# Optimization experiments

Hardware: AMD Instinct MI355X
Metric: run time of the kernel (lower is better)

The kernel has to match this reference:

```python
import jax, jax.numpy as jnp
import numpy as np

V = 32000; D = 1024; L = 2; H = 16; KVH = 4; HD = D // H; E = 8; FF = 2048; K = 2
B = 2; S = 1024; WINDOW = 4096; THETA = 10000.0; EPS = 1e-6


def setup_inputs() -> dict:
    key = jax.random.key(0)
    ks = jax.random.split(key, 12)
    std = 0.02
    return {
        'tokens': jax.random.randint(ks[0], (B, S), 0, V),
        'tok_emb': jax.random.normal(ks[1], (V, D), jnp.float32),  # nn.Embedding default N(0,1)
        'norm1_w': jnp.ones((L, D), jnp.float32),
        'norm2_w': jnp.ones((L, D), jnp.float32),
        'wq': jax.random.normal(ks[2], (L, D, D), jnp.float32) * std,
        'wk': jax.random.normal(ks[3], (L, KVH * HD, D), jnp.float32) * std,
        'wv': jax.random.normal(ks[4], (L, KVH * HD, D), jnp.float32) * std,
        'wo': jax.random.normal(ks[5], (L, D, D), jnp.float32) * std,
        'router_w': jax.random.normal(ks[6], (L, E, D), jnp.float32) * (std / np.sqrt(D)),
        'w1': jax.random.normal(ks[7], (L, E, FF, D), jnp.float32) * std,
        'w2': jax.random.normal(ks[8], (L, E, FF, D), jnp.float32) * std,
        'w3': jax.random.normal(ks[9], (L, E, D, FF), jnp.float32) * std,
        'normf_w': jnp.ones((D,), jnp.float32),
        'head_w': jax.random.normal(ks[10], (V, D), jnp.float32) * std,
    }


def rmsnorm(x, w):
    # F.normalize(x, dim=-1, eps) * w * sqrt(d)
    n = jnp.linalg.norm(x, axis=-1, keepdims=True)
    return x / jnp.maximum(n, EPS) * w * np.float32(np.sqrt(x.shape[-1]))


def rope(x, cos, sin):
    # x: (b, s, h, hd); pairs are interleaved (even, odd) per view_as_complex
    x2 = x.reshape(x.shape[:-1] + (-1, 2))
    x0, x1 = x2[..., 0], x2[..., 1]
    o0 = x0 * cos - x1 * sin
    o1 = x0 * sin + x1 * cos
    return jnp.stack([o0, o1], axis=-1).reshape(x.shape)


def attention(x, wq, wk, wv, wo, cos, sin):
    b, s, _ = x.shape
    q = (x @ wq.T).reshape(b, s, H, HD)
    k = (x @ wk.T).reshape(b, s, KVH, HD)
    v = (x @ wv.T).reshape(b, s, KVH, HD)
    q = rope(q, cos, sin)
    k = rope(k, cos, sin)
    g = H // KVH
    k = jnp.repeat(k, g, axis=2)
    v = jnp.repeat(v, g, axis=2)
    scores = jnp.einsum('bqhd,bkhd->bhqk', q, k) / np.float32(np.sqrt(HD))
    i = jnp.arange(s)[:, None]; j = jnp.arange(s)[None, :]
    allow = (j <= i) & (i - j < WINDOW)  # causal + sliding window
    scores = jnp.where(allow, scores, -jnp.inf)
    attn = jax.nn.softmax(scores, axis=-1)
    out = jnp.einsum('bhqk,bkhd->bqhd', attn, v).reshape(b, s, D)
    return out @ wo.T


def moe(x, router_w, w1, w2, w3):
    b, s, d = x.shape
    logits = jnp.einsum('bsd,ed->bse', x, router_w)
    probs = jax.nn.softmax(logits, axis=-1)
    _, idx = jax.lax.top_k(probs, K)                      # (b, s, K)
    mask = jax.nn.one_hot(idx, E, dtype=x.dtype).sum(-2)  # (b, s, E) binary
    xt = x.reshape(-1, d)           # (T, d)
    mt = mask.reshape(-1, E)        # (T, E)
    # Dense masked dispatch: every expert computed on all tokens, combine masks to zero
    u = jnp.einsum('td,efd->etf', xt, w1)
    g = jax.nn.silu(u) * jnp.einsum('td,efd->etf', xt, w2)
    y = jnp.einsum('etf,edf->etd', g, w3)
    out = jnp.einsum('etd,te->td', y, mt).reshape(b, s, d)  # unweighted combine (per source)
    # aux losses
    z_loss = jnp.mean(jax.scipy.special.logsumexp(logits, axis=-1)) ** 2
    load = probs.sum(axis=0)  # (s, E), matching probs.sum(dim=0) in source
    load_loss = (jnp.std(load, ddof=1) / jnp.mean(load)) ** 2
    aux = 0.001 * z_loss + 0.001 * load_loss
    return out, aux


def _rope_tables(dtype):
    freqs = 1.0 / (THETA ** (np.arange(0, HD, 2, dtype=np.float32) / HD))
    ang = np.arange(S, dtype=np.float32)[:, None] * freqs[None, :]
    cos = jnp.asarray(np.cos(ang), dtype)[None, :, None, :]
    sin = jnp.asarray(np.sin(ang), dtype)[None, :, None, :]
    return cos, sin


def reference(tokens, tok_emb, norm1_w, norm2_w, wq, wk, wv, wo, router_w, w1, w2, w3, normf_w, head_w):
    x = tok_emb[tokens]  # (B, S, D)
    cos, sin = _rope_tables(x.dtype)
    attn_scale = np.float32(1.0 / np.sqrt(2.0 * L))
    aux_total = jnp.zeros((), x.dtype)
    for l in range(L):
        x = x + attn_scale * attention(rmsnorm(x, norm1_w[l]), wq[l], wk[l], wv[l], wo[l], cos, sin)
        mo, aux = moe(rmsnorm(x, norm2_w[l]), router_w[l], w1[l], w2[l], w3[l])
        x = x + mo
        aux_total = aux_total + aux
    logits = rmsnorm(x, normf_w) @ head_w.T
    return logits, aux_total
```

## Files before the change

### kernel.cpp

```cpp
#include <hip/hip_runtime.h>
#include <math.h>

#define DEV __device__ __forceinline__

using v8s = __attribute__((ext_vector_type(8))) short;
using v4f = __attribute__((ext_vector_type(4))) float;

DEV short f2bf(float f) {
    unsigned u = __float_as_uint(f);
    unsigned r = (u + 0x7fffu + ((u >> 16) & 1u)) >> 16;
    return (short)(unsigned short)r;
}
DEV float bf2f(short s) {
    return __uint_as_float(((unsigned)(unsigned short)s) << 16);
}

DEV void gload16(const short* g, short* l) {
    __builtin_amdgcn_global_load_lds((const __attribute__((address_space(1))) void*)g,
                                     (__attribute__((address_space(3))) void*)l,
                                     16, 0, 0);
}

DEV void raw_barrier() { asm volatile("s_barrier" ::: "memory"); }

// ... 43 lines not shown
                                                     (unsigned short)l6, (unsigned short)l7);
        }
    }
}

struct GemmP {
    const short* Ah; const short* Al;
    const short* Bh; const short* Bl;
    float* C; short* Ch; short* Cl;
    const int* cnt; const int* ppd; const int* lrow;
    long aPanelsZ;
    long strideAz;
    long strideBz, strideCz;
    int M, N, K, lda, ldc;
    float alpha;
    int outMode;
    int gqaB;
    int grouped;
    int causalSkip;
    int causalK;
    int ntiles, S, G;
};

template<bool SPLIT, bool AREG>
__global__ __launch_bounds__(256) void gemm_bt(GemmP p) {
    const int lid = blockIdx.x;
    const int xcd = lid & 7, sI = lid >> 3;
    const int gi = xcd + 8 * (sI / p.S);
    if (gi >= p.G) return;
    const int mt = sI % p.S;
    const int nt = gi % p.ntiles;
    const int z  = gi / p.ntiles;
    if (p.causalSkip && nt > mt) return;

    const int tid = threadIdx.x;

    int Mz = p.grouped ? p.cnt[z] : p.M;
    if (mt * 128 >= Mz) return;

    long bOff;
    if (p.gqaB) { int b = z >> 4, h = z & 15; bOff = (long)(b * 4 + (h >> 2)) * p.strideBz; }
    else bOff = (long)z * p.strideBz;

    extern __shared__ char smem[];
    short* s0 = (short*)smem;
    const int BUF = SPLIT ? 16384 : 8192;

    const int lane = tid & 63, w = tid >> 6;
    const int lr = lane & 15, lg = lane >> 4;
    const int wr = w >> 1, wc = w & 1;

    v4f acc[4][4];
#pragma unroll
    for (int i = 0; i < 4; ++i)
#pragma unroll
        for (int j = 0; j < 4; ++j) { acc[i][j][0] = 0.f; acc[i][j][1] = 0.f; acc[i][j][2] = 0.f; acc[i][j][3] = 0.f; }

    const short* bks  = p.Bh + bOff + (long)nt * 128 * p.K + (long)w * 1024 + lane * 8;
    const short* bksL = SPLIT ? p.Bl + bOff + (long)nt * 128 * p.K + (long)w * 1024 + lane * 8 : nullptr;

    const short *aks = nullptr, *aksL = nullptr;
    const short *aH = nullptr, *aL = nullptr;
    short *sA0 = nullptr, *sA1 = nullptr, *sA0l = nullptr, *sA1l = nullptr;
    if constexpr (AREG) {
        const int r = tid & 127;
        const int kgA = tid >> 7;
        int am = mt * 128 + r; if (am >= Mz) am = Mz - 1;
        long arowoff = (long)z * p.strideAz + (long)am * p.lda;
        aH = p.Ah + arowoff + kgA * 16;
        aL = SPLIT ? p.Al + arowoff + kgA * 16 : nullptr;
        sA0 = s0 + (kgA * 256 + r) * 8; sA1 = sA0 + 1024;
        sA0l = s0 + 8192 + (kgA * 256 + r) * 8; sA1l = sA0l + 1024;
    } else {
        long aPanel = (p.grouped ? (long)(p.ppd[z] >> 7) : (long)z * p.aPanelsZ) + mt;
        aks  = p.Ah + aPanel * 128L * p.K + (long)w * 1024 + lane * 8;
        aksL = SPLIT ? p.Al + aPanel * 128L * p.K + (long)w * 1024 + lane * 8 : nullptr;
    }

    const int kEnd = p.causalK ? min(p.K, (mt + 1) * 128) : p.K;

    if constexpr (!AREG) {
        const int nIter = kEnd >> 5;
        const int wb = w * 1024;
        {
            const long kb = 0;
            short* base = s0;
            gload16(aks + kb,       base + wb);
            gload16(aks + kb + 512, base + wb + 512);
            gload16(bks + kb,       base + 4096 + wb);
            gload16(bks + kb + 512, base + 4096 + wb + 512);
            if (SPLIT) {
                gload16(aksL + kb,       base + 8192 + wb);
                gload16(aksL + kb + 512, base + 8192 + wb + 512);
                gload16(bksL + kb,       base + 12288 + wb);
                gload16(bksL + kb + 512, base + 12288 + wb + 512);
            }
        }
        for (int i = 0; i < nIter; ++i) {
            const int cur = i & 1;
            if (i + 1 < nIter) {
                raw_barrier();
                const long kb = (long)(i + 1) * 4096;
                short* base = s0 + (cur ^ 1) * BUF;
                gload16(aks + kb,       base + wb);
                gload16(aks + kb + 512, base + wb + 512);
                gload16(bks + kb,       base + 4096 + wb);
                gload16(bks + kb + 512, base + 4096 + wb + 512);
                if (SPLIT) {
                    gload16(aksL + kb,       base + 8192 + wb);
                    gload16(aksL + kb + 512, base + 8192 + wb + 512);
                    gload16(bksL + kb,       base + 12288 + wb);
                    gload16(bksL + kb + 512, base + 12288 + wb + 512);
                }
                if constexpr (SPLIT) asm volatile("s_waitcnt vmcnt(8)" ::: "memory");
                else                 asm volatile("s_waitcnt vmcnt(4)" ::: "memory");
            } else {
                asm volatile("s_waitcnt vmcnt(0)" ::: "memory");
            }
            raw_barrier();
            const short* base = s0 + cur * BUF;
            const int abase = lg * 1024 + (wr * 64 + lr) * 8;
            const int bbase = 4096 + lg * 1024 + (wc * 64 + lr) * 8;
            v8s ah[4], bh[4];
#pragma unroll
            for (int q = 0; q < 4; ++q) {
                ah[q] = *(const v8s*)(base + abase + q * 128);
                bh[q] = *(const v8s*)(base + bbase + q * 128);
            }
            if constexpr (SPLIT) {
                v8s al[4], bl[4];
#pragma unroll
                for (int q = 0; q < 4; ++q) {
                    al[q] = *(const v8s*)(base + 8192 + abase + q * 128);
                    bl[q] = *(const v8s*)(base + 8192 + bbase + q * 128);
                }
#pragma unroll
                for (int mi = 0; mi < 4; ++mi)
#pragma unroll
                    for (int nj = 0; nj < 4; ++nj) {
                        acc[mi][nj] = __builtin_amdgcn_mfma_f32_16x16x32_bf16(ah[mi], bh[nj], acc[mi][nj], 0, 0, 0);
                        acc[mi][nj] = __builtin_amdgcn_mfma_f32_16x16x32_bf16(al[mi], bh[nj], acc[mi][nj], 0, 0, 0);
                        acc[mi][nj] = __builtin_amdgcn_mfma_f32_16x16x32_bf16(ah[mi], bl[nj], acc[mi][nj], 0, 0, 0);
                    }
            } else {
#pragma unroll
                for (int mi = 0; mi < 4; ++mi)
#pragma unroll
                    for (int nj = 0; nj < 4; ++nj)
                        acc[mi][nj] = __builtin_amdgcn_mfma_f32_16x16x32_bf16(ah[mi], bh[nj], acc[mi][nj], 0, 0, 0);
            }
        }
    } else {
        short* Ahs = s0;
        short* Bhs = s0 + 4096;
        short* Als = s0 + 8192;
        short* Bls = s0 + 12288;
        const int wb = w * 1024;
        for (int k0 = 0; k0 < kEnd; k0 += 32) {
            const long kb = (long)k0 * 128;
            uint4 a0 = *(const uint4*)(aH + k0);
            uint4 a1 = *(const uint4*)(aH + k0 + 8);
            uint4 a0l, a1l;
            if (SPLIT) { a0l = *(const uint4*)(aL + k0); a1l = *(const uint4*)(aL + k0 + 8); }
            __syncthreads();
            gload16(bks + kb,       Bhs + wb);
            gload16(bks + kb + 512, Bhs + wb + 512);
            if (SPLIT) {
                gload16(bksL + kb,       Bls + wb);
                gload16(bksL + kb + 512, Bls + wb + 512);
            }
            *(uint4*)sA0 = a0; *(uint4*)sA1 = a1;
            if (SPLIT) { *(uint4*)sA0l = a0l; *(uint4*)sA1l = a1l; }
            __syncthreads();
            const int abase = lg * 1024 + (wr * 64 + lr) * 8;
            const int bbase = lg * 1024 + (wc * 64 + lr) * 8;
            v8s ah[4], bh[4];
#pragma unroll
            for (int q = 0; q < 4; ++q) {
                ah[q] = *(const v8s*)(Ahs + abase + q * 128);
                bh[q] = *(const v8s*)(Bhs + bbase + q * 128);
            }
            if constexpr (SPLIT) {
                v8s al[4], bl[4];
#pragma unroll
                for (int q = 0; q < 4; ++q) {
                    al[q] = *(const v8s*)(Als + abase + q * 128);
                    bl[q] = *(const v8s*)(Bls + bbase + q * 128);
                }
#pragma unroll
                for (int mi = 0; mi < 4; ++mi)
#pragma unroll
                    for (int nj = 0; nj < 4; ++nj) {
                        acc[mi][nj] = __builtin_amdgcn_mfma_f32_16x16x32_bf16(ah[mi], bh[nj], acc[mi][nj], 0, 0, 0);
                        acc[mi][nj] = __builtin_amdgcn_mfma_f32_16x16x32_bf16(al[mi], bh[nj], acc[mi][nj], 0, 0, 0);
                        acc[mi][nj] = __builtin_amdgcn_mfma_f32_16x16x32_bf16(ah[mi], bl[nj], acc[mi][nj], 0, 0, 0);
                    }
            } else {
#pragma unroll
                for (int mi = 0; mi < 4; ++mi)
#pragma unroll
                    for (int nj = 0; nj < 4; ++nj)
                        acc[mi][nj] = __builtin_amdgcn_mfma_f32_16x16x32_bf16(ah[mi], bh[nj], acc[mi][nj], 0, 0, 0);
            }
        }
    }

#pragma unroll
    for (int mi = 0; mi < 4; ++mi) {
        const int mrow = mt * 128 + wr * 64 + mi * 16 + lg * 4;
#pragma unroll
        for (int nj = 0; nj < 4; ++nj) {
            const int ncol = nt * 128 + wc * 64 + nj * 16 + lr;
            if (ncol < p.N) {
#pragma unroll
                for (int rr = 0; rr < 4; ++rr) {
                    const int m = mrow + rr;
                    if (m < Mz) {
                        float v = acc[mi][nj][rr] * p.alpha;
                        if (p.outMode == 3) {
                            int b = z >> 4, h = z & 15;
                            int grow = b * 1024 + m, col = h * 64 + ncol;
                            long dst = ((long)(grow >> 7)) * 131072 + ((long)(col >> 5) << 12)
                                     + ((long)((col >> 3) & 3) << 10) + ((long)(grow & 127) << 3) + (col & 7);
                            short hi = f2bf(v);
                            p.Ch[dst] = hi;
                            p.Cl[dst] = f2bf(v - bf2f(hi));
                        } else {
                            long crow;
                            if (p.grouped == 1)      crow = p.ppd[z] + m;
                            else if (p.grouped == 2) crow = p.lrow[z * 2048 + m];
                            else                     crow = m;
                            long co = (long)z * p.strideCz + crow * (long)p.ldc + ncol;
                            if (p.outMode == 0) p.C[co] = v;
                            else                p.C[co] += v;
                        }
                    }
                }
            }
        }
    }
}

__global__ __launch_bounds__(256) void embed_kernel(const int* toks, const float* emb, float* X) {
    const int t = blockIdx.x;
    const int tok = toks[t];
    const float4* s = (const float4*)(emb + (size_t)tok * 1024);
    float4* d = (float4*)(X + (size_t)t * 1024);
    d[threadIdx.x] = s[threadIdx.x];
}

__global__ __launch_bounds__(256) void rmsnorm_split(const float* X, const float* w, short* oh, short* ol) {
    __shared__ float red[4];
    const long t = blockIdx.x;
    const float* r = X + t * 1024;
    float ss = 0.f;
    for (int j = threadIdx.x; j < 1024; j += 256) { float f = r[j]; ss += f * f; }
    ss = block_sum256(ss, red);
    const float sc = 32.f / fmaxf(sqrtf(ss), 1e-6f);
    if (threadIdx.x < 128) {
// ... 45 lines not shown
    short h0 = f2bf(o0); KH[off] = h0; KL[off] = f2bf(o0 - bf2f(h0));
    short h1 = f2bf(o1); KH[off + 1] = h1; KL[off + 1] = f2bf(o1 - bf2f(h1));
}

__global__ __launch_bounds__(256) void transpose_v_kernel(const float* QKV, short* VH, short* VL) {
    const int idx = blockIdx.x * 256 + threadIdx.x;
    const int d = idx & 63, kv = (idx >> 6) & 3, s = (idx >> 8) & 1023, b = idx >> 18;
    const float f = QKV[((size_t)(b * 1024 + s)) * 1536 + 1280 + kv * 64 + d];
    const int z = b * 4 + kv;
    const long off = (long)z * 131072 + ((long)(s >> 5) << 12) + ((long)((s >> 3) & 3) << 10)
                   + ((long)d << 3) + (s & 7);
    short hi = f2bf(f);
    VH[off] = hi; VL[off] = f2bf(f - bf2f(hi));
    VH[off + 512] = 0; VL[off + 512] = 0;
}

__global__ __launch_bounds__(256) void attn_softmax(float* SC) {
    const long row = blockIdx.x;
    const int i = (int)(row & 1023);
    float* r = SC + row * 1024;
    __shared__ float buf[1024];
    __shared__ float red[4];
    const int n = i + 1;
    for (int j = threadIdx.x; j < 1024; j += 256) buf[j] = r[j];
    __syncthreads();
    float m = -INFINITY;
    for (int j = threadIdx.x; j < n; j += 256) m = fmaxf(m, buf[j]);
    m = block_max256(m, red);
    float s = 0.f;
    for (int j = threadIdx.x; j < n; j += 256) { float e = expf(buf[j] - m); buf[j] = e; s += e; }
    s = block_sum256(s, red);
    const float inv = 1.f / s;
    short* rh = (short*)r;
    short* rl = rh + 1024;
    __syncthreads();
    for (int j = threadIdx.x; j < 1024; j += 256) {
        float pv = (j < n) ? buf[j] * inv : 0.f;
        short hi = f2bf(pv);
        rh[j] = hi;
        rl[j] = f2bf(pv - bf2f(hi));
    }
}

__global__ __launch_bounds__(256) void router_kernel(const float* X, const float* wn, const float* rw,
                                                     float* probs, float* lse, int* cnt, int* ltok, int* lrow) {
    __shared__ float xs[1024];
    __shared__ float red[4];
// ... 19 lines not shown
    }
    __syncthreads();
    if (threadIdx.x == 0) {
        float m = lg[0];
        for (int e = 1; e < 8; ++e) m = fmaxf(m, lg[e]);
        float ex[8], se = 0.f;
        for (int e = 0; e < 8; ++e) { ex[e] = expf(lg[e] - m); se += ex[e]; }
        const float inv = 1.f / se;
        float pr[8];
        for (int e = 0; e < 8; ++e) { pr[e] = ex[e] * inv; probs[(size_t)t * 8 + e] = pr[e]; }
        lse[t] = m + logf(se);
        int i1 = 0;
        for (int e = 1; e < 8; ++e) if (pr[e] > pr[i1]) i1 = e;
        int i2 = (i1 == 0) ? 1 : 0;
        for (int e = 0; e < 8; ++e) if (e != i1 && pr[e] > pr[i2]) i2 = e;
        int s1 = atomicAdd(&cnt[i1], 1); ltok[i1 * 2048 + s1] = t; lrow[i1 * 2048 + s1] = 2 * t;
        int s2 = atomicAdd(&cnt[i2], 1); ltok[i2 * 2048 + s2] = t; lrow[i2 * 2048 + s2] = 2 * t + 1;
    }
}

__global__ void prefix_kernel(const int* cnt, int* ppd) {
    if (threadIdx.x == 0 && blockIdx.x == 0) {
        int a = 0;
        for (int e = 0; e < 8; ++e) { ppd[e] = a; a += ((cnt[e] + 127) >> 7) << 7; }
    }
}

__global__ __launch_bounds__(256) void gather_kernel(const short* XNH, const short* XNL,
                                                     const int* cnt, const int* ppd, const int* ltok,
                                                     short* GXNH, short* GXNL) {
    const int e = blockIdx.y, i = blockIdx.x;
    if (i >= cnt[e]) return;
    const int t = ltok[e * 2048 + i];
    const int pd = ppd[e] + i;
    const int plane = threadIdx.x >> 7, g = threadIdx.x & 127;
    const long goff = ((long)(g >> 2) << 12) + ((long)(g & 3) << 10);
    const long src = (long)(t >> 7) * 131072 + goff + ((t & 127) << 3);
    const long dst = (long)(pd >> 7) * 131072 + goff + ((pd & 127) << 3);
    const short* S = plane ? XNL : XNH;
    short* D = plane ? GXNL : GXNH;
    *(uint4*)(D + dst) = *(const uint4*)(S + src);
}

__global__ __launch_bounds__(256) void silu_mul(const float* U, short* HH, short* HL) {
    const int row = blockIdx.x, g = threadIdx.x;
    const float* ur = U + (long)row * 4096 + g * 8;
    const float4 u0 = *(const float4*)ur, u1 = *(const float4*)(ur + 4);
// ... 32 lines not shown
    float sl = 0.f;
    for (int t = threadIdx.x; t < 2048; t += 256) sl += lse[t];
    sl = block_sum256(sl, red);
    float s1 = 0.f, s2 = 0.f;
    for (int i = threadIdx.x; i < 8192; i += 256) {
        const float l = probs[i] + probs[8192 + i];
        s1 += l; s2 += l * l;
    }
    s1 = block_sum256(s1, red);
    s2 = block_sum256(s2, red);
    if (threadIdx.x == 0) {
        const float ml = sl / 2048.f;
        const float mean = s1 / 8192.f;
        const float var = fmaxf((s2 - s1 * s1 / 8192.f) / 8191.f, 0.f);
        auxb[layer] = 0.001f * (ml * ml + var / (mean * mean));
    }
}

__global__ void finalize_aux(const float* auxb, float* out) {
    if (threadIdx.x == 0 && blockIdx.x == 0)
        out[(size_t)2 * 1024 * 32000] = auxb[0] + auxb[1];
}

static void run_gemm(hipStream_t s, bool split, bool areg, GemmP& p, int ntiles, int mtiles, int zdim) {
    p.ntiles = ntiles; p.S = mtiles;
    p.G = ntiles * zdim;
    int Gp = (p.G + 7) & ~7;
    long nb = (long)Gp * mtiles;
    dim3 g((unsigned)nb, 1, 1), b(256);
    size_t lds = areg ? (split ? 32768 : 16384) : (split ? 65536 : 32768);
    if (split) {
        if (areg) gemm_bt<true, true><<<g, b, lds, s>>>(p);
        else      gemm_bt<true, false><<<g, b, lds, s>>>(p);
    } else {
        if (areg) gemm_bt<false, true><<<g, b, lds, s>>>(p);
        else      gemm_bt<false, false><<<g, b, lds, s>>>(p);
    }
}

static void run_tile(hipStream_t s, const float* src, short* hi, short* lo,
                     long rows, int K, long chunkRows, long chunkPanelStride) {
    long groups = rows * (K / 8);
    long nb = (groups + 255) / 256; if (nb > 2048) nb = 2048;
    conv_tile<<<(unsigned)nb, 256, 0, s>>>(src, hi, lo, groups, K / 8, chunkRows, chunkPanelStride);
}

extern "C" void kernel_launch(void* const* d_in, const int* in_sizes, int n_in,
                              void* d_out, int out_size, void* d_ws, size_t ws_size,
                              hipStream_t stream) {
    (void)in_sizes; (void)n_in; (void)out_size; (void)ws_size;
    const int*   tokens = (const int*)d_in[0];
    const float* tok_emb = (const float*)d_in[1];
    const float* norm1 = (const float*)d_in[2];
    const float* norm2 = (const float*)d_in[3];
    const float* wq = (const float*)d_in[4];
    const float* wk = (const float*)d_in[5];
    const float* wv = (const float*)d_in[6];
    const float* wo = (const float*)d_in[7];
    const float* rw = (const float*)d_in[8];
    const float* w1 = (const float*)d_in[9];
    const float* w2 = (const float*)d_in[10];
    const float* w3 = (const float*)d_in[11];
    const float* normf = (const float*)d_in[12];
    const float* headw = (const float*)d_in[13];
    float* out = (float*)d_out;

    char* w = (char*)d_ws;
    const size_t MB = 1024ull * 1024ull;
    float* X    = (float*)(w + 0);
    short* XNH  = (short*)(w + 8 * MB);
    short* XNL  = (short*)(w + 12 * MB);
    short* QRH  = (short*)(w + 16 * MB);
    short* QRL  = (short*)(w + 20 * MB);
    short* AOH  = QRH;
    short* AOL  = QRL;
    short* KRH  = (short*)(w + 24 * MB);
    short* KRL  = (short*)(w + 25 * MB);
    short* VTH  = (short*)(w + 26 * MB);
    short* VTL  = (short*)(w + 28 * MB);
    float* QKV  = (float*)(w + 32 * MB);
    float* SC   = (float*)(w + 32 * MB);
    float* U    = (float*)(w + 32 * MB);
    short* HH   = (short*)(w + 112 * MB);
    short* HL   = (short*)(w + 132 * MB);
    float* Y    = (float*)(w + 152 * MB);
    short* GXNH = (short*)(w + 168 * MB);
    short* GXNL = (short*)(w + 178 * MB);
    float* PROBS= (float*)(w + 188 * MB);
    float* LSE  = (float*)(w + 188 * MB + 65536);
    int*   CNT  = (int*)  (w + 188 * MB + 73728);
    int*   PPD  = (int*)  (w + 188 * MB + 73856);
    int*   LTOK = (int*)  (w + 188 * MB + 74240);
    int*   LROW = (int*)  (w + 188 * MB + 74240 + 65536);
    float* AUXB = (float*)(w + 188 * MB + 74240 + 131072);
    short* WQKVH = (short*)(w + 190 * MB);
    short* WQKVL = (short*)(w + 196 * MB);
    short* WOH   = (short*)(w + 202 * MB);
    short* WOL   = (short*)(w + 206 * MB);
    short* W12H  = (short*)(w + 210 * MB);
    short* W12L  = (short*)(w + 274 * MB);
    short* W3H   = (short*)(w + 338 * MB);
    short* W3L   = (short*)(w + 370 * MB);
    short* HDH   = (short*)(w + 274 * MB);

    RopeF rf;
    for (int i = 0; i < 32; ++i) {
        float t = (float)pow(10000.0, (double)(2 * i) / 64.0);
        rf.f[i] = 1.0f / t;
    }

    for (int l = 0; l < 2; ++l) {
        long qo = (long)l * 1572864;
        run_tile(stream, wq + (long)l * 1048576, WQKVH + qo,           WQKVL + qo,           1024, 1024, 1024, 8);
        run_tile(stream, wk + (long)l * 262144,  WQKVH + qo + 1048576, WQKVL + qo + 1048576, 256, 1024, 256, 2);
        run_tile(stream, wv + (long)l * 262144,  WQKVH + qo + 1310720, WQKVL + qo + 1310720, 256, 1024, 256, 2);
    }
    run_tile(stream, wo, WOH, WOL, 2048, 1024, 2048, 16);

    embed_kernel<<<2048, 256, 0, stream>>>(tokens, tok_emb, X);

    for (int l = 0; l < 2; ++l) {
        const bool msp = (l == 0);
        run_tile(stream, w1 + (long)l * 16777216, W12H,           msp ? W12L : nullptr,           16384, 1024, 2048, 32);
        run_tile(stream, w2 + (long)l * 16777216, W12H + 2097152, msp ? W12L + 2097152 : nullptr, 16384, 1024, 2048, 32);
        run_tile(stream, w3 + (long)l * 16777216, W3H,            msp ? W3L : nullptr,            8192, 2048, 8192, 64);

        rmsnorm_split<<<2048, 256, 0, stream>>>(X, norm1 + l * 1024, XNH, XNL);

        { GemmP p = {}; p.Ah = XNH; p.Al = XNL; p.Bh = WQKVH + (long)l * 1572864; p.Bl = WQKVL + (long)l * 1572864;
          p.C = QKV; p.M = 2048; p.N = 1536; p.K = 1024; p.aPanelsZ = 16; p.ldc = 1536; p.alpha = 1.f;
          run_gemm(stream, true, false, p, 12, 16, 1); }

        rope_q_kernel<<<4096, 256, 0, stream>>>(QKV, QRH, QRL, rf);
        rope_k_kernel<<<1024, 256, 0, stream>>>(QKV, KRH, KRL, rf);
        transpose_v_kernel<<<2048, 256, 0, stream>>>(QKV, VTH, VTL);

        { GemmP p = {}; p.Ah = QRH; p.Al = QRL; p.Bh = KRH; p.Bl = KRL; p.C = SC;
          p.M = 1024; p.N = 1024; p.K = 64; p.aPanelsZ = 8; p.ldc = 1024;
          p.strideBz = 65536; p.strideCz = 1048576;
          p.alpha = 0.125f; p.gqaB = 1; p.causalSkip = 1;
          run_gemm(stream, true, false, p, 8, 8, 32); }

        attn_softmax<<<32768, 256, 0, stream>>>(SC);

        { GemmP p = {}; p.Ah = (short*)SC; p.Al = (short*)SC + 1024; p.Bh = VTH; p.Bl = VTL; p.Ch = AOH; p.Cl = AOL;
          p.M = 1024; p.N = 64; p.K = 1024; p.lda = 2048;
          p.strideAz = 2097152; p.strideBz = 131072;
          p.alpha = 1.f; p.gqaB = 1; p.causalK = 1; p.outMode = 3;
          run_gemm(stream, true, true, p, 1, 8, 32); }

        { GemmP p = {}; p.Ah = AOH; p.Al = AOL; p.Bh = WOH + (long)l * 1048576; p.Bl = WOL + (long)l * 1048576; p.C = X;
          p.M = 2048; p.N = 1024; p.K = 1024; p.aPanelsZ = 16; p.ldc = 1024;
          p.alpha = 0.5f; p.outMode = 1;
          run_gemm(stream, true, false, p, 8, 16, 1); }

        rmsnorm_split<<<2048, 256, 0, stream>>>(X, norm2 + l * 1024, XNH, XNL);
        hipMemsetAsync(CNT, 0, 8 * sizeof(int), stream);
        router_kernel<<<2048, 256, 0, stream>>>(X, norm2 + l * 1024, rw + (size_t)l * 8 * 1024,
                                                PROBS, LSE, CNT, LTOK, LROW);
        prefix_kernel<<<1, 64, 0, stream>>>(CNT, PPD);
        { dim3 gg(2048, 8); gather_kernel<<<gg, 256, 0, stream>>>(XNH, XNL, CNT, PPD, LTOK, GXNH, GXNL); }

        { GemmP p = {}; p.Ah = GXNH; p.Al = GXNL; p.Bh = W12H; p.Bl = W12L; p.C = U;
          p.M = 2048; p.N = 4096; p.K = 1024; p.ldc = 4096;
          p.strideBz = 4194304; p.strideCz = 0; p.alpha = 1.f; p.grouped = 1;
          p.cnt = CNT; p.ppd = PPD; p.lrow = LROW;
          run_gemm(stream, msp, false, p, 32, 16, 8); }
        silu_mul<<<5120, 256, 0, stream>>>(U, HH, HL);
        { GemmP p = {}; p.Ah = HH; p.Al = HL; p.Bh = W3H; p.Bl = W3L; p.C = Y;
          p.M = 2048; p.N = 1024; p.K = 2048; p.ldc = 1024;
          p.strideBz = 2097152; p.strideCz = 0; p.alpha = 1.f; p.grouped = 2;
          p.cnt = CNT; p.ppd = PPD; p.lrow = LROW;
          run_gemm(stream, msp, false, p, 8, 16, 8); }
        combine_kernel<<<2048, 256, 0, stream>>>(X, Y);
        aux_kernel<<<1, 256, 0, stream>>>(PROBS, LSE, AUXB, l);

        if (l == 0)
            run_tile(stream, headw, HDH, nullptr, 32000, 1024, 32000, 250);
    }

    rmsnorm_split<<<2048, 256, 0, stream>>>(X, normf, XNH, XNL);
    { GemmP p = {}; p.Ah = XNH; p.Bh = HDH; p.C = out;
      p.M = 2048; p.N = 32000; p.K = 1024; p.aPanelsZ = 16; p.ldc = 32000; p.alpha = 1.f;
      run_gemm(stream, false, false, p, 250, 16, 1); }
    finalize_aux<<<1, 1, 0, stream>>>(AUXB, out);
}
```

Measured before the change: 2.209 ms.

## Add 256-row GEMM tile kernel and dedicated PV kernel, pad experts to 256

Adds a 512-thread GEMM variant that computes 256x128 output tiles, so each B tile loaded into LDS is reused across twice as many A rows. It is used for QK scores, the MoE up and down projections, and the LM head. The expert padding granularity moves to 256 and buffer offsets are reshuffled to fit. The AREG path is split out into a dedicated gemm_pv kernel, and the softmax now only loads the needed row prefix. Larger tiles cut B traffic but raise LDS use and padding waste, and they shrink the grid, which may lower occupancy and parallelism.

```diff
diff --git a/kernel.cpp b/kernel.cpp
--- a/kernel.cpp
+++ b/kernel.cpp
@@ -89,8 +89,8 @@
     int ntiles, S, G;
 };
 
-template<bool SPLIT, bool AREG>
-__global__ __launch_bounds__(256) void gemm_bt(GemmP p) {
+template<bool SPLIT>
+__global__ __launch_bounds__(256) void gemm_bt128(GemmP p) {
     const int lid = blockIdx.x;
     const int xcd = lid & 7, sI = lid >> 3;
     const int gi = xcd + 8 * (sI / p.S);
@@ -101,7 +101,6 @@
     if (p.causalSkip && nt > mt) return;
 
     const int tid = threadIdx.x;
-
     int Mz = p.grouped ? p.cnt[z] : p.M;
     if (mt * 128 >= Mz) return;
 
@@ -109,8 +108,7 @@
     if (p.gqaB) { int b = z >> 4, h = z & 15; bOff = (long)(b * 4 + (h >> 2)) * p.strideBz; }
     else bOff = (long)z * p.strideBz;
 
-    extern __shared__ char smem[];
-    short* s0 = (short*)smem;
+    extern __shared__ short s0[];
     const int BUF = SPLIT ? 16384 : 8192;
 
     const int lane = tid & 63, w = tid >> 6;
@@ -126,32 +124,30 @@
     const short* bks  = p.Bh + bOff + (long)nt * 128 * p.K + (long)w * 1024 + lane * 8;
     const short* bksL = SPLIT ? p.Bl + bOff + (long)nt * 128 * p.K + (long)w * 1024 + lane * 8 : nullptr;
 
-    const short *aks = nullptr, *aksL = nullptr;
-    const short *aH = nullptr, *aL = nullptr;
-    short *sA0 = nullptr, *sA1 = nullptr, *sA0l = nullptr, *sA1l = nullptr;
-    if constexpr (AREG) {
-        const int r = tid & 127;
-        const int kgA = tid >> 7;
-        int am = mt * 128 + r; if (am >= Mz) am = Mz - 1;
-        long arowoff = (long)z * p.strideAz + (long)am * p.lda;
-        aH = p.Ah + arowoff + kgA * 16;
-        aL = SPLIT ? p.Al + arowoff + kgA * 16 : nullptr;
-        sA0 = s0 + (kgA * 256 + r) * 8; sA1 = sA0 + 1024;
-        sA0l = s0 + 8192 + (kgA * 256 + r) * 8; sA1l = sA0l + 1024;
-    } else {
-        long aPanel = (p.grouped ? (long)(p.ppd[z] >> 7) : (long)z * p.aPanelsZ) + mt;
-        aks  = p.Ah + aPanel * 128L * p.K + (long)w * 1024 + lane * 8;
-        aksL = SPLIT ? p.Al + aPanel * 128L * p.K + (long)w * 1024 + lane * 8 : nullptr;
-    }
-
-    const int kEnd = p.causalK ? min(p.K, (mt + 1) * 128) : p.K;
-
-    if constexpr (!AREG) {
-        const int nIter = kEnd >> 5;
-        const int wb = w * 1024;
-        {
-            const long kb = 0;
-            short* base = s0;
+    long aPanel = (p.grouped ? (long)(p.ppd[z] >> 7) : (long)z * p.aPanelsZ) + mt;
+    const short* aks  = p.Ah + aPanel * 128L * p.K + (long)w * 1024 + lane * 8;
+    const short* aksL = SPLIT ? p.Al + aPanel * 128L * p.K + (long)w * 1024 + lane * 8 : nullptr;
+
+    const int nIter = p.K >> 5;
+    const int wb = w * 1024;
+    {
+        gload16(aks,       s0 + wb);
+        gload16(aks + 512, s0 + wb + 512);
+        gload16(bks,       s0 + 4096 + wb);
+        gload16(bks + 512, s0 + 4096 + wb + 512);
+        if (SPLIT) {
+            gload16(aksL,       s0 + 8192 + wb);
+            gload16(aksL + 512, s0 + 8192 + wb + 512);
+            gload16(bksL,       s0 + 12288 + wb);
+            gload16(bksL + 512, s0 + 12288 + wb + 512);
+        }
+    }
+    for (int i = 0; i < nIter; ++i) {
+        const int cur = i & 1;
+        if (i + 1 < nIter) {
+            raw_barrier();
+            const long kb = (long)(i + 1) * 4096;
+            short* base = s0 + (cur ^ 1) * BUF;
             gload16(aks + kb,       base + wb);
             gload16(aks + kb + 512, base + wb + 512);
             gload16(bks + kb,       base + 4096 + wb);
@@ -162,113 +158,42 @@
                 gload16(bksL + kb,       base + 12288 + wb);
                 gload16(bksL + kb + 512, base + 12288 + wb + 512);
             }
-        }
-        for (int i = 0; i < nIter; ++i) {
-            const int cur = i & 1;
-            if (i + 1 < nIter) {
-                raw_barrier();
-                const long kb = (long)(i + 1) * 4096;
-                short* base = s0 + (cur ^ 1) * BUF;
-                gload16(aks + kb,       base + wb);
-                gload16(aks + kb + 512, base + wb + 512);
-                gload16(bks + kb,       base + 4096 + wb);
-                gload16(bks + kb + 512, base + 4096 + wb + 512);
-                if (SPLIT) {
-                    gload16(aksL + kb,       base + 8192 + wb);
-                    gload16(aksL + kb + 512, base + 8192 + wb + 512);
-                    gload16(bksL + kb,       base + 12288 + wb);
-                    gload16(bksL + kb + 512, base + 12288 + wb + 512);
+            if constexpr (SPLIT) asm volatile("s_waitcnt vmcnt(8)" ::: "memory");
+            else                 asm volatile("s_waitcnt vmcnt(4)" ::: "memory");
+        } else {
+            asm volatile("s_waitcnt vmcnt(0)" ::: "memory");
+        }
+        raw_barrier();
+        const short* base = s0 + cur * BUF;
+        const int abase = lg * 1024 + (wr * 64 + lr) * 8;
+        const int bbase = 4096 + lg * 1024 + (wc * 64 + lr) * 8;
+        v8s ah[4], bh[4];
+#pragma unroll
+        for (int q = 0; q < 4; ++q) {
+            ah[q] = *(const v8s*)(base + abase + q * 128);
+            bh[q] = *(const v8s*)(base + bbase + q * 128);
+        }
+        if constexpr (SPLIT) {
+            v8s al[4], bl[4];
+#pragma unroll
+            for (int q = 0; q < 4; ++q) {
+                al[q] = *(const v8s*)(base + 8192 + abase + q * 128);
+                bl[q] = *(const v8s*)(base + 8192 + bbase + q * 128);
+            }
+#pragma unroll
+            for (int mi = 0; mi < 4; ++mi)
+#pragma unroll
+                for (int nj = 0; nj < 4; ++nj) {
+                    acc[mi][nj] = __builtin_amdgcn_mfma_f32_16x16x32_bf16(ah[mi], bh[nj], acc[mi][nj], 0, 0, 0);
+                    acc[mi][nj] = __builtin_amdgcn_mfma_f32_16x16x32_bf16(al[mi], bh[nj], acc[mi][nj], 0, 0, 0);
+                    acc[mi][nj] = __builtin_amdgcn_mfma_f32_16x16x32_bf16(ah[mi], bl[nj], acc[mi][nj], 0, 0, 0);
                 }
-                if constexpr (SPLIT) asm volatile("s_waitcnt vmcnt(8)" ::: "memory");
-                else                 asm volatile("s_waitcnt vmcnt(4)" ::: "memory");
-            } else {
-                asm volatile("s_waitcnt vmcnt(0)" ::: "memory");
-            }
-            raw_barrier();
-            const short* base = s0 + cur * BUF;
-            const int abase = lg * 1024 + (wr * 64 + lr) * 8;
-            const int bbase = 4096 + lg * 1024 + (wc * 64 + lr) * 8;
-            v8s ah[4], bh[4];
-#pragma unroll
-            for (int q = 0; q < 4; ++q) {
-                ah[q] = *(const v8s*)(base + abase + q * 128);
-                bh[q] = *(const v8s*)(base + bbase + q * 128);
-            }
-            if constexpr (SPLIT) {
-                v8s al[4], bl[4];
-#pragma unroll
-                for (int q = 0; q < 4; ++q) {
-                    al[q] = *(const v8s*)(base + 8192 + abase + q * 128);
-                    bl[q] = *(const v8s*)(base + 8192 + bbase + q * 128);
-                }
-#pragma unroll
-                for (int mi = 0; mi < 4; ++mi)
-#pragma unroll
-                    for (int nj = 0; nj < 4; ++nj) {
-                        acc[mi][nj] = __builtin_amdgcn_mfma_f32_16x16x32_bf16(ah[mi], bh[nj], acc[mi][nj], 0, 0, 0);
-                        acc[mi][nj] = __builtin_amdgcn_mfma_f32_16x16x32_bf16(al[mi], bh[nj], acc[mi][nj], 0, 0, 0);
-                        acc[mi][nj] = __builtin_amdgcn_mfma_f32_16x16x32_bf16(ah[mi], bl[nj], acc[mi][nj], 0, 0, 0);
-                    }
-            } else {
-#pragma unroll
-                for (int mi = 0; mi < 4; ++mi)
-#pragma unroll
-                    for (int nj = 0; nj < 4; ++nj)
-                        acc[mi][nj] = __builtin_amdgcn_mfma_f32_16x16x32_bf16(ah[mi], bh[nj], acc[mi][nj], 0, 0, 0);
-            }
-        }
-    } else {
-        short* Ahs = s0;
-        short* Bhs = s0 + 4096;
-        short* Als = s0 + 8192;
-        short* Bls = s0 + 12288;
-        const int wb = w * 1024;
-        for (int k0 = 0; k0 < kEnd; k0 += 32) {
-            const long kb = (long)k0 * 128;
-            uint4 a0 = *(const uint4*)(aH + k0);
-            uint4 a1 = *(const uint4*)(aH + k0 + 8);
-            uint4 a0l, a1l;
-            if (SPLIT) { a0l = *(const uint4*)(aL + k0); a1l = *(const uint4*)(aL + k0 + 8); }
-            __syncthreads();
-            gload16(bks + kb,       Bhs + wb);
-            gload16(bks + kb + 512, Bhs + wb + 512);
-            if (SPLIT) {
-                gload16(bksL + kb,       Bls + wb);
-                gload16(bksL + kb + 512, Bls + wb + 512);
-            }
-            *(uint4*)sA0 = a0; *(uint4*)sA1 = a1;
-            if (SPLIT) { *(uint4*)sA0l = a0l; *(uint4*)sA1l = a1l; }
-            __syncthreads();
-            const int abase = lg * 1024 + (wr * 64 + lr) * 8;
-            const int bbase = lg * 1024 + (wc * 64 + lr) * 8;
-            v8s ah[4], bh[4];
-#pragma unroll
-            for (int q = 0; q < 4; ++q) {
-                ah[q] = *(const v8s*)(Ahs + abase + q * 128);
-                bh[q] = *(const v8s*)(Bhs + bbase + q * 128);
-            }
-            if constexpr (SPLIT) {
-                v8s al[4], bl[4];
-#pragma unroll
-                for (int q = 0; q < 4; ++q) {
-                    al[q] = *(const v8s*)(Als + abase + q * 128);
-                    bl[q] = *(const v8s*)(Bls + bbase + q * 128);
-                }
-#pragma unroll
-                for (int mi = 0; mi < 4; ++mi)
-#pragma unroll
-                    for (int nj = 0; nj < 4; ++nj) {
-                        acc[mi][nj] = __builtin_amdgcn_mfma_f32_16x16x32_bf16(ah[mi], bh[nj], acc[mi][nj], 0, 0, 0);
-                        acc[mi][nj] = __builtin_amdgcn_mfma_f32_16x16x32_bf16(al[mi], bh[nj], acc[mi][nj], 0, 0, 0);
-                        acc[mi][nj] = __builtin_amdgcn_mfma_f32_16x16x32_bf16(ah[mi], bl[nj], acc[mi][nj], 0, 0, 0);
-                    }
-            } else {
-#pragma unroll
-                for (int mi = 0; mi < 4; ++mi)
-#pragma unroll
-                    for (int nj = 0; nj < 4; ++nj)
-                        acc[mi][nj] = __builtin_amdgcn_mfma_f32_16x16x32_bf16(ah[mi], bh[nj], acc[mi][nj], 0, 0, 0);
-            }
+        } else {
+#pragma unroll
+            for (int mi = 0; mi < 4; ++mi)
+#pragma unroll
+                for (int nj = 0; nj < 4; ++nj)
+                    acc[mi][nj] = __builtin_amdgcn_mfma_f32_16x16x32_bf16(ah[mi], bh[nj], acc[mi][nj], 0, 0, 0);
         }
     }
 
@@ -284,24 +209,247 @@
                     const int m = mrow + rr;
                     if (m < Mz) {
                         float v = acc[mi][nj][rr] * p.alpha;
-                        if (p.outMode == 3) {
-                            int b = z >> 4, h = z & 15;
-                            int grow = b * 1024 + m, col = h * 64 + ncol;
-                            long dst = ((long)(grow >> 7)) * 131072 + ((long)(col >> 5) << 12)
-                                     + ((long)((col >> 3) & 3) << 10) + ((long)(grow & 127) << 3) + (col & 7);
-                            short hi = f2bf(v);
-                            p.Ch[dst] = hi;
-                            p.Cl[dst] = f2bf(v - bf2f(hi));
-                        } else {
-                            long crow;
-                            if (p.grouped == 1)      crow = p.ppd[z] + m;
-                            else if (p.grouped == 2) crow = p.lrow[z * 2048 + m];
-                            else                     crow = m;
-                            long co = (long)z * p.strideCz + crow * (long)p.ldc + ncol;
-                            if (p.outMode == 0) p.C[co] = v;
-                            else                p.C[co] += v;
-                        }
+                        long crow;
+                        if (p.grouped == 1)      crow = p.ppd[z] + m;
+                        else if (p.grouped == 2) crow = p.lrow[z * 2048 + m];
+                        else                     crow = m;
+                        long co = (long)z * p.strideCz + crow * (long)p.ldc + ncol;
+                        if (p.outMode == 0) p.C[co] = v;
+                        else                p.C[co] += v;
                     }
+                }
+            }
+        }
+    }
+}
+
+template<bool SPLIT>
+__global__ __launch_bounds__(512) void gemm_bt256(GemmP p) {
+    const int lid = blockIdx.x;
+    const int xcd = lid & 7, sI = lid >> 3;
+    const int gi = xcd + 8 * (sI / p.S);
+    if (gi >= p.G) return;
+    const int mt = sI % p.S;
+    const int nt = gi % p.ntiles;
+    const int z  = gi / p.ntiles;
+    if (p.causalSkip && nt > 2 * mt + 1) return;
+
+    const int tid = threadIdx.x;
+    int Mz = p.grouped ? p.cnt[z] : p.M;
+    if (mt * 256 >= Mz) return;
+
+    long bOff;
+    if (p.gqaB) { int b = z >> 4, h = z & 15; bOff = (long)(b * 4 + (h >> 2)) * p.strideBz; }
+    else bOff = (long)z * p.strideBz;
+
+    extern __shared__ short s0[];
+    const int BUF = SPLIT ? 24576 : 12288;
+
+    const int lane = tid & 63, w = tid >> 6;
+    const int lr = lane & 15, lg = lane >> 4;
+    const int wr = w >> 1, wc = w & 1;
+
+    v4f acc[4][4];
+#pragma unroll
+    for (int i = 0; i < 4; ++i)
+#pragma unroll
+        for (int j = 0; j < 4; ++j) { acc[i][j][0] = 0.f; acc[i][j][1] = 0.f; acc[i][j][2] = 0.f; acc[i][j][3] = 0.f; }
+
+    const short* bks  = p.Bh + bOff + (long)nt * 128 * p.K + (long)w * 512 + lane * 8;
+    const short* bksL = SPLIT ? p.Bl + bOff + (long)nt * 128 * p.K + (long)w * 512 + lane * 8 : nullptr;
+    const long aPanelBase = (p.grouped ? (long)(p.ppd[z] >> 7) : (long)z * p.aPanelsZ) + 2L * mt;
+    const int u0 = 2 * w, u1 = 2 * w + 1;
+    const short* aks0  = p.Ah + (aPanelBase + (u0 >> 3)) * 128L * p.K + (long)(u0 & 7) * 512 + lane * 8;
+    const short* aks1  = p.Ah + (aPanelBase + (u1 >> 3)) * 128L * p.K + (long)(u1 & 7) * 512 + lane * 8;
+    const short* aks0L = SPLIT ? p.Al + (aPanelBase + (u0 >> 3)) * 128L * p.K + (long)(u0 & 7) * 512 + lane * 8 : nullptr;
+    const short* aks1L = SPLIT ? p.Al + (aPanelBase + (u1 >> 3)) * 128L * p.K + (long)(u1 & 7) * 512 + lane * 8 : nullptr;
+    short* dA0 = s0 + u0 * 512;
+    short* dA1 = s0 + u1 * 512;
+    short* dB  = s0 + 8192 + w * 512;
+
+    const int nIter = p.K >> 5;
+    {
+        gload16(aks0, dA0);
+        gload16(aks1, dA1);
+        gload16(bks,  dB);
+        if (SPLIT) {
+            gload16(aks0L, dA0 + 12288);
+            gload16(aks1L, dA1 + 12288);
+            gload16(bksL,  dB + 12288);
+        }
+    }
+    for (int i = 0; i < nIter; ++i) {
+        const int cur = i & 1;
+        if (i + 1 < nIter) {
+            raw_barrier();
+            const long kb = (long)(i + 1) * 4096;
+            const int boff = (cur ^ 1) * BUF;
+            gload16(aks0 + kb, dA0 + boff);
+            gload16(aks1 + kb, dA1 + boff);
+            gload16(bks + kb,  dB + boff);
+            if (SPLIT) {
+                gload16(aks0L + kb, dA0 + boff + 12288);
+                gload16(aks1L + kb, dA1 + boff + 12288);
+                gload16(bksL + kb,  dB + boff + 12288);
+            }
+            if constexpr (SPLIT) asm volatile("s_waitcnt vmcnt(6)" ::: "memory");
+            else                 asm volatile("s_waitcnt vmcnt(3)" ::: "memory");
+        } else {
+            asm volatile("s_waitcnt vmcnt(0)" ::: "memory");
+        }
+        raw_barrier();
+        const short* base = s0 + cur * BUF;
+        const int abase = (wr >> 1) * 4096 + lg * 1024 + ((wr & 1) * 64 + lr) * 8;
+        const int bbase = 8192 + lg * 1024 + (wc * 64 + lr) * 8;
+        v8s ah[4], bh[4];
+#pragma unroll
+        for (int q = 0; q < 4; ++q) {
+            ah[q] = *(const v8s*)(base + abase + q * 128);
+            bh[q] = *(const v8s*)(base + bbase + q * 128);
+        }
+        if constexpr (SPLIT) {
+            v8s al[4], bl[4];
+#pragma unroll
+            for (int q = 0; q < 4; ++q) {
+                al[q] = *(const v8s*)(base + 12288 + abase + q * 128);
+                bl[q] = *(const v8s*)(base + 12288 + bbase + q * 128);
+            }
+#pragma unroll
+            for (int mi = 0; mi < 4; ++mi)
+#pragma unroll
+                for (int nj = 0; nj < 4; ++nj) {
+                    acc[mi][nj] = __builtin_amdgcn_mfma_f32_16x16x32_bf16(ah[mi], bh[nj], acc[mi][nj], 0, 0, 0);
+                    acc[mi][nj] = __builtin_amdgcn_mfma_f32_16x16x32_bf16(al[mi], bh[nj], acc[mi][nj], 0, 0, 0);
+                    acc[mi][nj] = __builtin_amdgcn_mfma_f32_16x16x32_bf16(ah[mi], bl[nj], acc[mi][nj], 0, 0, 0);
+                }
+        } else {
+#pragma unroll
+            for (int mi = 0; mi < 4; ++mi)
+#pragma unroll
+                for (int nj = 0; nj < 4; ++nj)
+                    acc[mi][nj] = __builtin_amdgcn_mfma_f32_16x16x32_bf16(ah[mi], bh[nj], acc[mi][nj], 0, 0, 0);
+        }
+    }
+
+#pragma unroll
+    for (int mi = 0; mi < 4; ++mi) {
+        const int mrow = mt * 256 + wr * 64 + mi * 16 + lg * 4;
+#pragma unroll
+        for (int nj = 0; nj < 4; ++nj) {
+            const int ncol = nt * 128 + wc * 64 + nj * 16 + lr;
+            if (ncol < p.N) {
+#pragma unroll
+                for (int rr = 0; rr < 4; ++rr) {
+                    const int m = mrow + rr;
+                    if (m < Mz) {
+                        float v = acc[mi][nj][rr] * p.alpha;
+                        long crow;
+                        if (p.grouped == 1)      crow = p.ppd[z] + m;
+                        else if (p.grouped == 2) crow = p.lrow[z * 2048 + m];
+                        else                     crow = m;
+                        long co = (long)z * p.strideCz + crow * (long)p.ldc + ncol;
+                        if (p.outMode == 0) p.C[co] = v;
+                        else                p.C[co] += v;
+                    }
+                }
+            }
+        }
+    }
+}
+
+__global__ __launch_bounds__(256) void gemm_pv(GemmP p) {
+    const int lid = blockIdx.x;
+    const int xcd = lid & 7, sI = lid >> 3;
+    const int gi = xcd + 8 * (sI / p.S);
+    if (gi >= p.G) return;
+    const int mt = sI % p.S;
+    const int z  = gi;
+    const int tid = threadIdx.x;
+
+    const int b = z >> 4, h = z & 15;
+    const long bOff = (long)(b * 4 + (h >> 2)) * p.strideBz;
+
+    extern __shared__ short s0[];
+    short* Ahs = s0;
+    short* Bhs = s0 + 4096;
+    short* Als = s0 + 8192;
+    short* Bls = s0 + 12288;
+
+    const int lane = tid & 63, w = tid >> 6;
+    const int lr = lane & 15, lg = lane >> 4;
+    const int wr = w >> 1, wc = w & 1;
+
+    v4f acc[4][4];
+#pragma unroll
+    for (int i = 0; i < 4; ++i)
+#pragma unroll
+        for (int j = 0; j < 4; ++j) { acc[i][j][0] = 0.f; acc[i][j][1] = 0.f; acc[i][j][2] = 0.f; acc[i][j][3] = 0.f; }
+
+    const short* bks  = p.Bh + bOff + (long)w * 1024 + lane * 8;
+    const short* bksL = p.Bl + bOff + (long)w * 1024 + lane * 8;
+
+    const int r = tid & 127;
+    const int kgA = tid >> 7;
+    const int am = mt * 128 + r;
+    const long arowoff = (long)z * p.strideAz + (long)am * p.lda;
+    const short* aH = p.Ah + arowoff + kgA * 16;
+    const short* aL = p.Al + arowoff + kgA * 16;
+    short* sA0 = s0 + (kgA * 256 + r) * 8; short* sA1 = sA0 + 1024;
+    short* sA0l = s0 + 8192 + (kgA * 256 + r) * 8; short* sA1l = sA0l + 1024;
+
+    const int kEnd = min(p.K, (mt + 1) * 128);
+    const int wb = w * 1024;
+    for (int k0 = 0; k0 < kEnd; k0 += 32) {
+        const long kb = (long)k0 * 128;
+        uint4 a0 = *(const uint4*)(aH + k0);
+        uint4 a1 = *(const uint4*)(aH + k0 + 8);
+        uint4 a0l = *(const uint4*)(aL + k0);
+        uint4 a1l = *(const uint4*)(aL + k0 + 8);
+        __syncthreads();
+        gload16(bks + kb,       Bhs + wb);
+        gload16(bks + kb + 512, Bhs + wb + 512);
+        gload16(bksL + kb,       Bls + wb);
+        gload16(bksL + kb + 512, Bls + wb + 512);
+        *(uint4*)sA0 = a0; *(uint4*)sA1 = a1;
+        *(uint4*)sA0l = a0l; *(uint4*)sA1l = a1l;
+        __syncthreads();
+        const int abase = lg * 1024 + (wr * 64 + lr) * 8;
+        const int bbase = lg * 1024 + (wc * 64 + lr) * 8;
+        v8s ah[4], bh[4], al[4], bl[4];
+#pragma unroll
+        for (int q = 0; q < 4; ++q) {
+            ah[q] = *(const v8s*)(Ahs + abase + q * 128);
+            bh[q] = *(const v8s*)(Bhs + bbase + q * 128);
+            al[q] = *(const v8s*)(Als + abase + q * 128);
+            bl[q] = *(const v8s*)(Bls + bbase + q * 128);
+        }
+#pragma unroll
+        for (int mi = 0; mi < 4; ++mi)
+#pragma unroll
+            for (int nj = 0; nj < 4; ++nj) {
+                acc[mi][nj] = __builtin_amdgcn_mfma_f32_16x16x32_bf16(ah[mi], bh[nj], acc[mi][nj], 0, 0, 0);
+                acc[mi][nj] = __builtin_amdgcn_mfma_f32_16x16x32_bf16(al[mi], bh[nj], acc[mi][nj], 0, 0, 0);
+                acc[mi][nj] = __builtin_amdgcn_mfma_f32_16x16x32_bf16(ah[mi], bl[nj], acc[mi][nj], 0, 0, 0);
+            }
+    }
+
+#pragma unroll
+    for (int mi = 0; mi < 4; ++mi) {
+        const int mrow = mt * 128 + wr * 64 + mi * 16 + lg * 4;
+#pragma unroll
+        for (int nj = 0; nj < 4; ++nj) {
+            const int ncol = wc * 64 + nj * 16 + lr;
+            if (ncol < 64) {
+#pragma unroll
+                for (int rr = 0; rr < 4; ++rr) {
+                    const int m = mrow + rr;
+                    float v = acc[mi][nj][rr];
+                    int grow = b * 1024 + m, col = h * 64 + ncol;
+                    long dst = ((long)(grow >> 7)) * 131072 + ((long)(col >> 5) << 12)
+                             + ((long)((col >> 3) & 3) << 10) + ((long)(grow & 127) << 3) + (col & 7);
+                    short hi = f2bf(v);
+                    p.Ch[dst] = hi;
+                    p.Cl[dst] = f2bf(v - bf2f(hi));
                 }
             }
         }
@@ -393,7 +541,7 @@
     __shared__ float buf[1024];
     __shared__ float red[4];
     const int n = i + 1;
-    for (int j = threadIdx.x; j < 1024; j += 256) buf[j] = r[j];
+    for (int j = threadIdx.x; j < n; j += 256) buf[j] = r[j];
     __syncthreads();
     float m = -INFINITY;
     for (int j = threadIdx.x; j < n; j += 256) m = fmaxf(m, buf[j]);
@@ -459,7 +607,7 @@
 __global__ void prefix_kernel(const int* cnt, int* ppd) {
     if (threadIdx.x == 0 && blockIdx.x == 0) {
         int a = 0;
-        for (int e = 0; e < 8; ++e) { ppd[e] = a; a += ((cnt[e] + 127) >> 7) << 7; }
+        for (int e = 0; e < 8; ++e) { ppd[e] = a; a += ((cnt[e] + 255) >> 8) << 8; }
     }
 }
 
@@ -538,20 +686,24 @@
         out[(size_t)2 * 1024 * 32000] = auxb[0] + auxb[1];
 }
 
-static void run_gemm(hipStream_t s, bool split, bool areg, GemmP& p, int ntiles, int mtiles, int zdim) {
+static void run_gemm128(hipStream_t s, bool split, GemmP& p, int ntiles, int mtiles, int zdim) {
     p.ntiles = ntiles; p.S = mtiles;
     p.G = ntiles * zdim;
     int Gp = (p.G + 7) & ~7;
     long nb = (long)Gp * mtiles;
     dim3 g((unsigned)nb, 1, 1), b(256);
-    size_t lds = areg ? (split ? 32768 : 16384) : (split ? 65536 : 32768);
-    if (split) {
-        if (areg) gemm_bt<true, true><<<g, b, lds, s>>>(p);
-        else      gemm_bt<true, false><<<g, b, lds, s>>>(p);
-    } else {
-        if (areg) gemm_bt<false, true><<<g, b, lds, s>>>(p);
-        else      gemm_bt<false, false><<<g, b, lds, s>>>(p);
-    }
+    if (split) gemm_bt128<true><<<g, b, 65536, s>>>(p);
+    else       gemm_bt128<false><<<g, b, 32768, s>>>(p);
+}
+
+static void run_gemm256(hipStream_t s, bool split, GemmP& p, int ntiles, int mtiles, int zdim) {
+    p.ntiles = ntiles; p.S = mtiles;
+    p.G = ntiles * zdim;
+    int Gp = (p.G + 7) & ~7;
+    long nb = (long)Gp * mtiles;
+    dim3 g((unsigned)nb, 1, 1), b(512);
+    if (split) gemm_bt256<true><<<g, b, 98304, s>>>(p);
+    else       gemm_bt256<false><<<g, b, 49152, s>>>(p);
 }
 
 static void run_tile(hipStream_t s, const float* src, short* hi, short* lo,
@@ -596,28 +748,28 @@
     short* VTL  = (short*)(w + 28 * MB);
     float* QKV  = (float*)(w + 32 * MB);
     float* SC   = (float*)(w + 32 * MB);
-    float* U    = (float*)(w + 32 * MB);
-    short* HH   = (short*)(w + 112 * MB);
-    short* HL   = (short*)(w + 132 * MB);
-    float* Y    = (float*)(w + 152 * MB);
-    short* GXNH = (short*)(w + 168 * MB);
-    short* GXNL = (short*)(w + 178 * MB);
-    float* PROBS= (float*)(w + 188 * MB);
-    float* LSE  = (float*)(w + 188 * MB + 65536);
-    int*   CNT  = (int*)  (w + 188 * MB + 73728);
-    int*   PPD  = (int*)  (w + 188 * MB + 73856);
-    int*   LTOK = (int*)  (w + 188 * MB + 74240);
-    int*   LROW = (int*)  (w + 188 * MB + 74240 + 65536);
-    float* AUXB = (float*)(w + 188 * MB + 74240 + 131072);
-    short* WQKVH = (short*)(w + 190 * MB);
-    short* WQKVL = (short*)(w + 196 * MB);
-    short* WOH   = (short*)(w + 202 * MB);
-    short* WOL   = (short*)(w + 206 * MB);
-    short* W12H  = (short*)(w + 210 * MB);
-    short* W12L  = (short*)(w + 274 * MB);
-    short* W3H   = (short*)(w + 338 * MB);
-    short* W3L   = (short*)(w + 370 * MB);
-    short* HDH   = (short*)(w + 274 * MB);
+    short* GXNH = (short*)(w + 32 * MB);
+    short* GXNL = (short*)(w + 44 * MB);
+    float* U    = (float*)(w + 56 * MB);
+    short* HH   = (short*)(w + 152 * MB);
+    short* HL   = (short*)(w + 176 * MB);
+    float* Y    = (float*)(w + 200 * MB);
+    float* PROBS= (float*)(w + 216 * MB);
+    float* LSE  = (float*)(w + 216 * MB + 65536);
+    int*   CNT  = (int*)  (w + 216 * MB + 73728);
+    int*   PPD  = (int*)  (w + 216 * MB + 73856);
+    int*   LTOK = (int*)  (w + 216 * MB + 74240);
+    int*   LROW = (int*)  (w + 216 * MB + 74240 + 65536);
+    float* AUXB = (float*)(w + 216 * MB + 74240 + 131072);
+    short* WQKVH = (short*)(w + 218 * MB);
+    short* WQKVL = (short*)(w + 224 * MB);
+    short* WOH   = (short*)(w + 230 * MB);
+    short* WOL   = (short*)(w + 234 * MB);
+    short* W12H  = (short*)(w + 238 * MB);
+    short* W12L  = (short*)(w + 302 * MB);
+    short* W3H   = (short*)(w + 366 * MB);
+    short* W3L   = (short*)(w + 398 * MB);
+    short* HDH   = (short*)(w + 302 * MB);
 
     RopeF rf;
     for (int i = 0; i < 32; ++i) {
@@ -645,7 +797,7 @@
 
         { GemmP p = {}; p.Ah = XNH; p.Al = XNL; p.Bh = WQKVH + (long)l * 1572864; p.Bl = WQKVL + (long)l * 1572864;
           p.C = QKV; p.M = 2048; p.N = 1536; p.K = 1024; p.aPanelsZ = 16; p.ldc = 1536; p.alpha = 1.f;
-          run_gemm(stream, true, false, p, 12, 16, 1); }
+          run_gemm128(stream, true, p, 12, 16, 1); }
 
         rope_q_kernel<<<4096, 256, 0, stream>>>(QKV, QRH, QRL, rf);
         rope_k_kernel<<<1024, 256, 0, stream>>>(QKV, KRH, KRL, rf);
@@ -655,20 +807,21 @@
           p.M = 1024; p.N = 1024; p.K = 64; p.aPanelsZ = 8; p.ldc = 1024;
           p.strideBz = 65536; p.strideCz = 1048576;
           p.alpha = 0.125f; p.gqaB = 1; p.causalSkip = 1;
-          run_gemm(stream, true, false, p, 8, 8, 32); }
+          run_gemm256(stream, true, p, 8, 4, 32); }
 
         attn_softmax<<<32768, 256, 0, stream>>>(SC);
 
         { GemmP p = {}; p.Ah = (short*)SC; p.Al = (short*)SC + 1024; p.Bh = VTH; p.Bl = VTL; p.Ch = AOH; p.Cl = AOL;
           p.M = 1024; p.N = 64; p.K = 1024; p.lda = 2048;
           p.strideAz = 2097152; p.strideBz = 131072;
-          p.alpha = 1.f; p.gqaB = 1; p.causalK = 1; p.outMode = 3;
-          run_gemm(stream, true, true, p, 1, 8, 32); }
+          p.ntiles = 1; p.S = 8; p.G = 32;
+          long nb = 32L * 8;
+          gemm_pv<<<dim3((unsigned)nb), dim3(256), 32768, stream>>>(p); }
 
         { GemmP p = {}; p.Ah = AOH; p.Al = AOL; p.Bh = WOH + (long)l * 1048576; p.Bl = WOL + (long)l * 1048576; p.C = X;
           p.M = 2048; p.N = 1024; p.K = 1024; p.aPanelsZ = 16; p.ldc = 1024;
           p.alpha = 0.5f; p.outMode = 1;
-          run_gemm(stream, true, false, p, 8, 16, 1); }
+          run_gemm128(stream, true, p, 8, 16, 1); }
 
         rmsnorm_split<<<2048, 256, 0, stream>>>(X, norm2 + l * 1024, XNH, XNL);
         hipMemsetAsync(CNT, 0, 8 * sizeof(int), stream);
@@ -681,13 +834,13 @@
           p.M = 2048; p.N = 4096; p.K = 1024; p.ldc = 4096;
           p.strideBz = 4194304; p.strideCz = 0; p.alpha = 1.f; p.grouped = 1;
           p.cnt = CNT; p.ppd = PPD; p.lrow = LROW;
-          run_gemm(stream, msp, false, p, 32, 16, 8); }
-        silu_mul<<<5120, 256, 0, stream>>>(U, HH, HL);
+          run_gemm256(stream, msp, p, 32, 8, 8); }
+        silu_mul<<<6144, 256, 0, stream>>>(U, HH, HL);
         { GemmP p = {}; p.Ah = HH; p.Al = HL; p.Bh = W3H; p.Bl = W3L; p.C = Y;
           p.M = 2048; p.N = 1024; p.K = 2048; p.ldc = 1024;
           p.strideBz = 2097152; p.strideCz = 0; p.alpha = 1.f; p.grouped = 2;
           p.cnt = CNT; p.ppd = PPD; p.lrow = LROW;
-          run_gemm(stream, msp, false, p, 8, 16, 8); }
+          run_gemm256(stream, msp, p, 8, 8, 8); }
         combine_kernel<<<2048, 256, 0, stream>>>(X, Y);
         aux_kernel<<<1, 256, 0, stream>>>(PROBS, LSE, AUXB, l);
 
@@ -698,6 +851,6 @@
     rmsnorm_split<<<2048, 256, 0, stream>>>(X, normf, XNH, XNL);
     { GemmP p = {}; p.Ah = XNH; p.Bh = HDH; p.C = out;
       p.M = 2048; p.N = 32000; p.K = 1024; p.aPanelsZ = 16; p.ldc = 32000; p.alpha = 1.f;
-      run_gemm(stream, false, false, p, 250, 16, 1); }
+      run_gemm256(stream, false, p, 250, 8, 1); }
     finalize_aux<<<1, 1, 0, stream>>>(AUXB, out);
 }
```

Measured after the change: 2.164 ms. -2.1%, faster.
